# Optimization experiments

Hardware: AMD Instinct MI355X
Metric: run time of the kernel (lower is better)

The kernel has to match this reference:

```python
import jax, jax.numpy as jnp
import numpy as np
from jax import lax

B, S, D, H = 512, 120, 216, 1024
MAX_LEN = 24


def setup_inputs() -> dict:
    key = jax.random.key(0)
    ks = jax.random.split(key, 8)
    u = lambda k, shape: jax.random.uniform(k, shape, jnp.float32, -0.08, 0.08)  # init_weights
    return {
        "src": jax.random.normal(ks[0], (B, S, D), jnp.float32),
        "W_ih": u(ks[1], (4 * H, D)),
        "W_hh": u(ks[2], (4 * H, H)),
        "b_ih": u(ks[3], (4 * H,)),
        "b_hh": u(ks[4], (4 * H,)),
        "W_out": u(ks[5], (D, H)),
        "b_out": u(ks[6], (D,)),
        "max_len": MAX_LEN,
    }


def _lstm_cell(x, h, c, W_ih, W_hh, b):
    # PyTorch gate order: i, f, g, o
    gates = x @ W_ih.T + h @ W_hh.T + b  # (B, 4H)
    i, f, g, o = jnp.split(gates, 4, axis=-1)
    c_new = jax.nn.sigmoid(f) * c + jax.nn.sigmoid(i) * jnp.tanh(g)
    h_new = jax.nn.sigmoid(o) * jnp.tanh(c_new)
    return h_new, c_new


def reference(src, W_ih, W_hh, b_ih, b_hh, W_out, b_out, max_len):
    # Eval-mode forward: dropout off; encoder teacher-forced over src;
    b = b_ih + b_hh
    src_t = jnp.swapaxes(src, 0, 1)  # (S, B, D)
    Bsz = src.shape[0]
    Hd = W_hh.shape[1]
    h0 = jnp.zeros((Bsz, Hd), src.dtype)
    c0 = jnp.zeros((Bsz, Hd), src.dtype)

    def enc_step(carry, x_t):
        h, c = carry
        h, c = _lstm_cell(x_t, h, c, W_ih, W_hh, b)
        return (h, c), None

    (h, c), _ = lax.scan(enc_step, (h0, c0), src_t)

    def dec_step(carry, _):
        h, c, inp = carry
        h, c = _lstm_cell(inp, h, c, W_ih, W_hh, b)
        y = h @ W_out.T + b_out  # project_to_output
        return (h, c, y), y

    (_, _, _), ys = lax.scan(dec_step, (h, c, src_t[-1]), None, length=max_len)
    return jnp.swapaxes(ys, 0, 1)  # (B, max_len, D)
```

## Files before the change

kernel.cpp:

```cpp
#include <hip/hip_runtime.h>
#include <cstdint>
#include <cstddef>

#define B_SZ 512
#define S_SZ 120
#define D_SZ 216
#define H_SZ 1024
#define NG   4096
#define DP   256
#define TMAX 24

#define BM 64
#define BN 128
#define BK 64

using bf16_t = __bf16;
using bf16x8 = __attribute__((ext_vector_type(8))) __bf16;
using f32x4  = __attribute__((ext_vector_type(4))) float;

__device__ __forceinline__ void gload16(const void* g, void* l) {
  __builtin_amdgcn_global_load_lds(
      (const __attribute__((address_space(1))) void*)g,
      (__attribute__((address_space(3))) void*)l, 16, 0, 0);
}

__device__ __forceinline__ float fsigmoid(float x) {
  x = fminf(fmaxf(x, -30.f), 30.f);
  return 1.f / (1.f + __expf(-x));
}
__device__ __forceinline__ float ftanh(float x) {
  x = fminf(fmaxf(x, -15.f), 15.f);
  float e = __expf(2.f * x);
  return (e - 1.f) / (e + 1.f);
}

struct __align__(16) Smem {
  union {
    bf16_t bufs[2][6 * 64 * 64];
    struct { char pad[49152]; float gate[64 * 129]; } g;
  };
};


template <int EPI, int N1, int N2>
__global__ __launch_bounds__(256, 1) void gemm_step(
    const bf16_t* __restrict__ A1, int sA1,
    const bf16_t* __restrict__ A2, int sA2,
    const bf16_t* __restrict__ Wsw,
    const float* __restrict__ bias,
    float* __restrict__ cbuf, bf16_t* __restrict__ hout,
    const float* __restrict__ addm, bf16_t* __restrict__ outb,
    float* __restrict__ outf)
{
  constexpr int NTOT = N1 + N2;
  constexpr int KB   = NTOT * 2;
  constexpr int C0 = NTOT < 4 ? NTOT : 4;
  constexpr int R0 = NTOT - C0;
  constexpr int C1 = R0 < 6 ? R0 : 6;
  constexpr int R1 = R0 - C1;
  constexpr int C2 = R1 < 6 ? R1 : 6;
  constexpr int C3 = R1 - C2;
  static_assert(C3 <= 6, "chunk overflow");

  __shared__ Smem sm;
  const int t    = threadIdx.x;
  const int m0   = blockIdx.y * BM;
  const int n0   = blockIdx.x * BN;
  const int lane = t & 63;
  const int wv   = t >> 6;
  const int fr   = lane & 15;
  const int fq   = lane >> 4;

  f32x4 acc[4][2] = {};

  float bias2[2] = {0.f, 0.f};
  if (EPI == 1 || EPI == 3) {
#pragma unroll
    for (int nj = 0; nj < 2; ++nj) {
      int col = n0 + wv * 32 + nj * 16 + fr;
      bias2[nj] = (EPI == 3 && col >= D_SZ) ? 0.f : bias[col];
    }
  }

  auto stageChunk = [&](int ci, int kst, int csz) {
    const bf16_t* Ap; int sA; int kloc;
    if (ci == 0 && N1 > 0) { Ap = A1; sA = sA1; kloc = 0; }
    else                   { Ap = A2; sA = sA2; kloc = kst - N1 * BK; }
    char* base = (char*)&sm.bufs[ci & 1][0];
    const int row8 = t >> 3;
    const int c16s = (t & 7);
#pragma unroll
    for (int half = 0; half < 2; ++half) {
      int row = half * 32 + row8;
      int gc  = (c16s ^ (row & 7)) * 8;
      const bf16_t* ga = Ap + (size_t)(m0 + row) * sA + kloc + gc;
      char* ldst = base + (half * 32 + wv * 8) * 128;
      for (int seg = 0; seg < csz; ++seg)
        gload16(ga + seg * 64, ldst + seg * 8192);
    }
  };

  const int nb0 = (n0 >> 4) + wv * 2;
  auto loadB = [&](int it, bf16x8* Bv) {
#pragma unroll
    for (int nj = 0; nj < 2; ++nj)
#pragma unroll
      for (int kk = 0; kk < 2; ++kk)
        Bv[nj * 2 + kk] = *(const bf16x8*)((const char*)Wsw +
            ((size_t)((nb0 + nj) * KB + it * 2 + kk) * 64 + lane) * 16);
  };

  auto compute = [&](const bf16x8* Bv, int bufi, int seg) {
    const char* base = (const char*)&sm.bufs[bufi][0] + seg * 8192;
#pragma unroll
    for (int kk = 0; kk < 2; ++kk)
#pragma unroll
      for (int mi = 0; mi < 4; ++mi) {
        int row = mi * 16 + fr;
        bf16x8 av = *(const bf16x8*)(base + row * 128 +
                                     (((kk * 4 + fq) ^ (row & 7)) * 16));
        acc[mi][0] = __builtin_amdgcn_mfma_f32_16x16x32_bf16(av, Bv[kk],     acc[mi][0], 0, 0, 0);
        acc[mi][1] = __builtin_amdgcn_mfma_f32_16x16x32_bf16(av, Bv[2 + kk], acc[mi][1], 0, 0, 0);
      }
  };

  bf16x8 Bv[2][4];
  loadB(0, Bv[0]);
  stageChunk(0, 0, C0);
  __syncthreads();
  if (C1 > 0) stageChunk(1, C0 * BK, C1);
#pragma unroll
  for (int i = 0; i < C0; ++i) {
    if (i + 1 < NTOT) loadB(i + 1, Bv[(i + 1) & 1]);
    compute(Bv[i & 1], 0, i);
  }
  if (C1 > 0) {
    __syncthreads();
    if (C2 > 0) stageChunk(2, (C0 + C1) * BK, C2);
#pragma unroll
    for (int i = 0; i < C1; ++i) {
      int it = C0 + i;
      if (it + 1 < NTOT) loadB(it + 1, Bv[(it + 1) & 1]);
      compute(Bv[it & 1], 1, i);
    }
  }
  if (C2 > 0) {
    __syncthreads();
    if (C3 > 0) stageChunk(3, (C0 + C1 + C2) * BK, C3);
#pragma unroll
    for (int i = 0; i < C2; ++i) {
      int it = C0 + C1 + i;
      if (it + 1 < NTOT) loadB(it + 1, Bv[(it + 1) & 1]);
      compute(Bv[it & 1], 0, i);
    }
  }
  if (C3 > 0) {
    __syncthreads();
#pragma unroll
    for (int i = 0; i < C3; ++i) {
      int it = C0 + C1 + C2 + i;
      if (it + 1 < NTOT) loadB(it + 1, Bv[(it + 1) & 1]);
      compute(Bv[it & 1], 1, i);
    }
  }
  __syncthreads();

  if (EPI == 1) {
#pragma unroll
    for (int mi = 0; mi < 4; ++mi)
#pragma unroll
      for (int nj = 0; nj < 2; ++nj)
#pragma unroll
        for (int v = 0; v < 4; ++v) {
          int row = mi * 16 + fq * 4 + v;
          int col = wv * 32 + nj * 16 + fr;
          sm.g.gate[row * 129 + col] = acc[mi][nj][v] + bias2[nj];
        }
    __syncthreads();
    const int u0 = n0 >> 2;
#pragma unroll
    for (int itc = 0; itc < 8; ++itc) {
      int ci = itc * 256 + t;
      int brw = ci >> 5;
      int ju  = ci & 31;
      const float* gp = &sm.g.gate[brw * 129 + ju * 4];
      float iv = fsigmoid(gp[0]);
      float fv = fsigmoid(gp[1]);
      float gv = ftanh(gp[2]);
      float ov = fsigmoid(gp[3]);
      size_t cix = (size_t)(m0 + brw) * H_SZ + (u0 + ju);
      float cn = fv * cbuf[cix] + iv * gv;
      cbuf[cix] = cn;
      hout[cix] = (bf16_t)(ov * ftanh(cn));
    }
  }

  if (EPI == 2) {
#pragma unroll
    for (int mi = 0; mi < 4; ++mi)
#pragma unroll
      for (int nj = 0; nj < 2; ++nj)
#pragma unroll
        for (int v = 0; v < 4; ++v) {
          int row = mi * 16 + fq * 4 + v;
          int col = wv * 32 + nj * 16 + fr;
          int gr = m0 + row, gc = n0 + col;
          int orig = (gr & 3) * H_SZ + (gr >> 2);
          sm.g.gate[row * 129 + col] = acc[mi][nj][v] + addm[(size_t)orig * H_SZ + gc];
        }
    __syncthreads();
#pragma unroll
    for (int q = 0; q < 4; ++q) {
      int c = q * 256 + t;
      int nbl = c >> 8, kbl = (c >> 6) & 3, l2 = c & 63;
      int nloc = nbl * 16 + (l2 & 15);
      int kloc = kbl * 32 + (l2 >> 4) * 8;
      const float* gp = &sm.g.gate[nloc * 129 + kloc];
      bf16x8 v;
#pragma unroll
      for (int j = 0; j < 8; ++j) v[j] = (bf16_t)gp[j];
      size_t chunk = (size_t)(((m0 >> 4) + nbl) * 32 + (n0 >> 5) + kbl) * 64 + l2;
      *(bf16x8*)(outb + chunk * 8) = v;
    }
  }

  if (EPI == 3) {
#pragma unroll
    for (int mi = 0; mi < 4; ++mi)
#pragma unroll
      for (int nj = 0; nj < 2; ++nj)
#pragma unroll
        for (int v = 0; v < 4; ++v) {
          int m = m0 + mi * 16 + fq * 4 + v;
          int n = n0 + wv * 32 + nj * 16 + fr;
          if (n < D_SZ) {
            outf[((size_t)(m & 511) * TMAX + (m >> 9)) * D_SZ + n] =
                acc[mi][nj][v] + bias2[nj];
          }
        }
  }
}

__global__ void k_convert_src(const float* __restrict__ src, bf16_t* __restrict__ dst) {
  int idx = blockIdx.x * 256 + threadIdx.x;
  int total = S_SZ * B_SZ * DP;
  if (idx >= total) return;
  int d = idx % DP;
  int r = idx / DP;
  int b = r % B_SZ;
  int tt = r / B_SZ;
  float v = (d < D_SZ) ? src[((size_t)b * S_SZ + tt) * D_SZ + d] : 0.f;
  dst[idx] = (bf16_t)v;
}

__global__ void k_build_wcat_sw(const float* __restrict__ Wih, const float* __restrict__ Whh,
                                bf16_t* __restrict__ out) {
  int c = blockIdx.x * 256 + threadIdx.x;
  if (c >= 256 * 40 * 64) return;
  int l = c & 63;
  int kb = (c >> 6) % 40;
  int nb = c / (40 * 64);
  int n = nb * 16 + (l & 15);
  int k0 = kb * 32 + (l >> 4) * 8;
  int o = (n & 3) * H_SZ + (n >> 2);
  bf16x8 v;
#pragma unroll
  for (int j = 0; j < 8; ++j) {
    int k = k0 + j;
    float x = (k < D_SZ) ? Wih[(size_t)o * D_SZ + k]
            : (k < DP ? 0.f : Whh[(size_t)o * H_SZ + (k - DP)]);
    v[j] = (bf16_t)x;
  }
  *(bf16x8*)(out + (size_t)c * 8) = v;
}

__global__ void k_build_woutt_sw(const float* __restrict__ Wout, bf16_t* __restrict__ out) {
  int c = blockIdx.x * 256 + threadIdx.x;
  if (c >= 64 * 8 * 64) return;
  int l = c & 63;
  int kb = (c >> 6) % 8;
  int nb = c / (8 * 64);
  int n = nb * 16 + (l & 15);
  int k0 = kb * 32 + (l >> 4) * 8;
  bf16x8 v;
#pragma unroll
  for (int j = 0; j < 8; ++j) {
    int k = k0 + j;
    v[j] = (bf16_t)((k < D_SZ) ? Wout[(size_t)k * H_SZ + n] : 0.f);
  }
  *(bf16x8*)(out + (size_t)c * 8) = v;
}

__global__ void k_build_wout_sw(const float* __restrict__ Wout, bf16_t* __restrict__ out) {
  int c = blockIdx.x * 256 + threadIdx.x;
  if (c >= 16 * 32 * 64) return;
  int l = c & 63;
  int kb = (c >> 6) % 32;
  int nb = c / (32 * 64);
  int n = nb * 16 + (l & 15);
  int k0 = kb * 32 + (l >> 4) * 8;
  bf16x8 v;
#pragma unroll
  for (int j = 0; j < 8; ++j)
    v[j] = (bf16_t)((n < D_SZ) ? Wout[(size_t)n * H_SZ + k0 + j] : 0.f);
  *(bf16x8*)(out + (size_t)c * 8) = v;
}

__global__ void k_build_wihre(const float* __restrict__ Wih, bf16_t* __restrict__ out) {
  int c = blockIdx.x * 256 + threadIdx.x;
  if (c >= 4096 * 32) return;
  int r = c >> 5;
  int k0 = (c & 31) * 8;
  int o = (r & 3) * H_SZ + (r >> 2);
  bf16x8 v;
#pragma unroll
  for (int j = 0; j < 8; ++j) {
    int k = k0 + j;
    v[j] = (bf16_t)((k < D_SZ) ? Wih[(size_t)o * D_SZ + k] : 0.f);
  }
  *(bf16x8*)(out + (size_t)c * 8) = v;
}

__global__ void k_build_bias(const float* __restrict__ bih, const float* __restrict__ bhh,
                             const float* __restrict__ Wih, const float* __restrict__ bout,
                             float* __restrict__ biasE, float* __restrict__ biasD) {
  int r = blockIdx.x * 256 + threadIdx.x;
  if (r >= NG) return;
  int o = (r & 3) * H_SZ + (r >> 2);
  float be = bih[o] + bhh[o];
  biasE[r] = be;
  float s = 0.f;
  const float* wr = Wih + (size_t)o * D_SZ;
  for (int d = 0; d < D_SZ; ++d) s += wr[d] * bout[d];
  biasD[r] = be + s;
}

extern "C" void kernel_launch(void* const* d_in, const int* in_sizes, int n_in,
                              void* d_out, int out_size, void* d_ws, size_t ws_size,
                              hipStream_t stream) {
  const float* src  = (const float*)d_in[0];
  const float* Wih  = (const float*)d_in[1];
  const float* Whh  = (const float*)d_in[2];
  const float* bih  = (const float*)d_in[3];
  const float* bhh  = (const float*)d_in[4];
  const float* Wout = (const float*)d_in[5];
  const float* bout = (const float*)d_in[6];

  char* ws = (char*)d_ws;
  size_t off = 0;
  auto alloc = [&](size_t bytes) {
    void* p = ws + off;
    off = (off + bytes + 255) & ~(size_t)255;
    return p;
  };
  bf16_t* srcbf  = (bf16_t*)alloc((size_t)S_SZ * B_SZ * DP * 2);
  bf16_t* WcatSw = (bf16_t*)alloc((size_t)256 * 40 * 64 * 16);
  bf16_t* WdecSw = (bf16_t*)alloc((size_t)NG * H_SZ * 2);
  bf16_t* WouttSw= (bf16_t*)alloc((size_t)64 * 8 * 64 * 16);
  bf16_t* WoutSw = (bf16_t*)alloc((size_t)16 * 32 * 64 * 16);
  bf16_t* WihRe  = (bf16_t*)alloc((size_t)NG * DP * 2);
  float*  biasE  = (float*)alloc((size_t)NG * 4);
  float*  biasD  = (float*)alloc((size_t)NG * 4);
  float*  cbuf   = (float*)alloc((size_t)B_SZ * H_SZ * 4);
  bf16_t* hP0    = (bf16_t*)alloc((size_t)B_SZ * H_SZ * 2);
  bf16_t* hP1    = (bf16_t*)alloc((size_t)B_SZ * H_SZ * 2);
  bf16_t* Hs     = (bf16_t*)alloc((size_t)TMAX * B_SZ * H_SZ * 2);

  hipMemsetAsync(cbuf, 0, (size_t)B_SZ * H_SZ * 4, stream);
  hipMemsetAsync(hP0, 0, (size_t)B_SZ * H_SZ * 2, stream);

  k_convert_src<<<(S_SZ * B_SZ * DP + 255) / 256, 256, 0, stream>>>(src, srcbf);
  k_build_wcat_sw<<<(256 * 40 * 64 + 255) / 256, 256, 0, stream>>>(Wih, Whh, WcatSw);
  k_build_woutt_sw<<<(64 * 8 * 64 + 255) / 256, 256, 0, stream>>>(Wout, WouttSw);
  k_build_wout_sw<<<(16 * 32 * 64 + 255) / 256, 256, 0, stream>>>(Wout, WoutSw);
  k_build_wihre<<<(4096 * 32 + 255) / 256, 256, 0, stream>>>(Wih, WihRe);
  k_build_bias<<<(NG + 255) / 256, 256, 0, stream>>>(bih, bhh, Wih, bout, biasE, biasD);

  gemm_step<2, 4, 0><<<dim3(H_SZ / BN, NG / BM), 256, 0, stream>>>(
      WihRe, DP, nullptr, 0, WouttSw, nullptr,
      nullptr, nullptr, Whh, WdecSw, nullptr);

  const bf16_t* hprev = hP0;
  for (int s = 0; s < 144; ++s) {
    bf16_t* hnext;
    if (s < 120) hnext = (hprev == hP0) ? hP1 : hP0;
    else         hnext = Hs + (size_t)(s - 120) * B_SZ * H_SZ;
    if (s <= 120) {
      int xi = (s <= 119) ? s : 119;
      gemm_step<1, 4, 16><<<dim3(NG / BN, B_SZ / BM), 256, 0, stream>>>(
          srcbf + (size_t)xi * B_SZ * DP, DP, hprev, H_SZ,
          WcatSw, biasE, cbuf, hnext, nullptr, nullptr, nullptr);
    } else {
      gemm_step<1, 0, 16><<<dim3(NG / BN, B_SZ / BM), 256, 0, stream>>>(
          nullptr, 0, hprev, H_SZ,
          WdecSw, biasD, cbuf, hnext, nullptr, nullptr, nullptr);
    }
    hprev = hnext;
  }

  gemm_step<3, 0, 16><<<dim3(2, (TMAX * B_SZ) / BM), 256, 0, stream>>>(
      nullptr, 0, Hs, H_SZ, WoutSw, bout,
      nullptr, nullptr, nullptr, nullptr, (float*)d_out);
}
```

Measured before the change: 2.023 ms.

## Replace per-step LSTM launches with persistent kernel using per-row-group barriers

Replaces the 144 per-timestep gemm_step launches with a single persistent kernel of 256 blocks. Blocks sync through atomic counters per batch-row group, so each block waits only on the 32 blocks producing its rows of h. The cell state now stays in registers instead of a global cbuf, and the x-projection for the next step is issued before the wait on h, so it overlaps the barrier. This removes launch overhead and global c traffic. In exchange it depends on all 256 blocks being co-resident, or the spin-waits deadlock, and it adds spin-wait and fence latency.

```diff
diff --git a/kernel.cpp b/kernel.cpp
--- a/kernel.cpp
+++ b/kernel.cpp
@@ -42,13 +42,176 @@
 };
 
 
+__global__ __launch_bounds__(256, 1) void lstm_persist(
+    const bf16_t* __restrict__ srcbf,
+    const bf16_t* __restrict__ WcatSw,
+    const bf16_t* __restrict__ WdecSw,
+    const float* __restrict__ biasE,
+    const float* __restrict__ biasD,
+    bf16_t* __restrict__ hP0, bf16_t* __restrict__ hP1,
+    bf16_t* __restrict__ Hs,
+    int* __restrict__ bars)
+{
+  __shared__ Smem sm;
+  const int t    = threadIdx.x;
+  const int nt   = blockIdx.x;
+  const int gI   = blockIdx.y;
+  const int m0   = gI * BM;
+  const int n0   = nt * BN;
+  const int lane = t & 63;
+  const int wv   = t >> 6;
+  const int fr   = lane & 15;
+  const int fq   = lane >> 4;
+  const int u0   = n0 >> 2;
+  const size_t BH = (size_t)B_SZ * H_SZ;
+
+  float bE[2], bD[2];
+#pragma unroll
+  for (int nj = 0; nj < 2; ++nj) {
+    int col = n0 + wv * 32 + nj * 16 + fr;
+    bE[nj] = biasE[col];
+    bD[nj] = biasD[col];
+  }
+
+  float creg[8];
+#pragma unroll
+  for (int i = 0; i < 8; ++i) creg[i] = 0.f;
+
+  const int nb0  = (n0 >> 4) + wv * 2;
+  const int row8 = t >> 3;
+  const int c16s = t & 7;
+
+  auto stageA = [&](const bf16_t* Ap, int sA, int buf, int k0, int nseg) {
+    char* base = (char*)&sm.bufs[0][0] + buf * 49152;
+#pragma unroll
+    for (int half = 0; half < 2; ++half) {
+      int row = half * 32 + row8;
+      int gc  = (c16s ^ (row & 7)) * 8;
+      const bf16_t* ga = Ap + (size_t)(m0 + row) * sA + k0 + gc;
+      char* ldst = base + (half * 32 + wv * 8) * 128;
+      for (int seg = 0; seg < nseg; ++seg)
+        gload16(ga + seg * 64, ldst + seg * 8192);
+    }
+  };
+
+  for (int s = 0; s < 144; ++s) {
+    const bool enc = (s <= 120);
+    const int  KBs = enc ? 40 : 32;
+    const bf16_t* Wb0 = (enc ? WcatSw : WdecSw) + (size_t)nb0 * KBs * 512;
+    const bf16_t* Wb1 = Wb0 + (size_t)KBs * 512;
+    const float*  b2  = enc ? bE : bD;
+    bf16_t* hw = (s < 120) ? ((s & 1) ? hP1 : hP0) : Hs + (size_t)(s - 120) * BH;
+    const bf16_t* hr = (s == 0) ? nullptr
+                     : (s - 1 < 120) ? (((s - 1) & 1) ? hP1 : hP0)
+                                     : Hs + (size_t)(s - 1 - 120) * BH;
+
+    f32x4 acc[4][2] = {};
+    bf16x8 Bv[2][4];
+
+    auto loadB = [&](int kb, bf16x8* B) {
+      B[0] = *(const bf16x8*)(Wb0 + (size_t)kb * 512 + lane * 8);
+      B[1] = *(const bf16x8*)(Wb0 + (size_t)(kb + 1) * 512 + lane * 8);
+      B[2] = *(const bf16x8*)(Wb1 + (size_t)kb * 512 + lane * 8);
+      B[3] = *(const bf16x8*)(Wb1 + (size_t)(kb + 1) * 512 + lane * 8);
+    };
+    auto compute = [&](int buf, int seg, const bf16x8* B) {
+      const char* base = (const char*)&sm.bufs[0][0] + buf * 49152 + seg * 8192;
+#pragma unroll
+      for (int kk = 0; kk < 2; ++kk)
+#pragma unroll
+        for (int mi = 0; mi < 4; ++mi) {
+          int row = mi * 16 + fr;
+          bf16x8 av = *(const bf16x8*)(base + row * 128 +
+                                       (((kk * 4 + fq) ^ (row & 7)) * 16));
+          acc[mi][0] = __builtin_amdgcn_mfma_f32_16x16x32_bf16(av, B[kk],     acc[mi][0], 0, 0, 0);
+          acc[mi][1] = __builtin_amdgcn_mfma_f32_16x16x32_bf16(av, B[2 + kk], acc[mi][1], 0, 0, 0);
+        }
+    };
+
+    int it = 0;
+    if (enc) {
+      int xi = (s <= 119) ? s : 119;
+      const bf16_t* As = srcbf + (size_t)xi * B_SZ * DP;
+      stageA(As, DP, 0, 0, 4);
+      loadB(0, Bv[0]);
+      __syncthreads();
+#pragma unroll
+      for (int i = 0; i < 4; ++i, ++it) {
+        loadB(2 * (it + 1), Bv[(it + 1) & 1]);
+        compute(0, i, Bv[it & 1]);
+      }
+    }
+    if (s > 0) {
+      if (t == 0) {
+        while (__hip_atomic_load(&bars[(s - 1) * 8 + gI], __ATOMIC_RELAXED,
+                                 __HIP_MEMORY_SCOPE_AGENT) < 32)
+          __builtin_amdgcn_s_sleep(2);
+      }
+      __syncthreads();
+      __threadfence();
+      stageA(hr, H_SZ, 1, 0, 6);
+      __syncthreads();
+      stageA(hr, H_SZ, 0, 384, 6);
+      if (!enc) loadB(2 * it, Bv[it & 1]);
+#pragma unroll
+      for (int i = 0; i < 6; ++i, ++it) {
+        loadB(2 * (it + 1), Bv[(it + 1) & 1]);
+        compute(1, i, Bv[it & 1]);
+      }
+      __syncthreads();
+      stageA(hr, H_SZ, 1, 768, 4);
+#pragma unroll
+      for (int i = 0; i < 6; ++i, ++it) {
+        loadB(2 * (it + 1), Bv[(it + 1) & 1]);
+        compute(0, i, Bv[it & 1]);
+      }
+      __syncthreads();
+#pragma unroll
+      for (int i = 0; i < 4; ++i, ++it) {
+        if (i < 3) loadB(2 * (it + 1), Bv[(it + 1) & 1]);
+        compute(1, i, Bv[it & 1]);
+      }
+    }
+
+    __syncthreads();
+#pragma unroll
+    for (int mi = 0; mi < 4; ++mi)
+#pragma unroll
+      for (int nj = 0; nj < 2; ++nj)
+#pragma unroll
+        for (int v = 0; v < 4; ++v) {
+          int row = mi * 16 + fq * 4 + v;
+          int col = wv * 32 + nj * 16 + fr;
+          sm.g.gate[row * 129 + col] = acc[mi][nj][v] + b2[nj];
+        }
+    __syncthreads();
+#pragma unroll
+    for (int itc = 0; itc < 8; ++itc) {
+      int brw = itc * 8 + (t >> 5);
+      int ju  = t & 31;
+      const float* gp = &sm.g.gate[brw * 129 + ju * 4];
+      float iv = fsigmoid(gp[0]);
+      float fv = fsigmoid(gp[1]);
+      float gv = ftanh(gp[2]);
+      float ov = fsigmoid(gp[3]);
+      float cn = fv * creg[itc] + iv * gv;
+      creg[itc] = cn;
+      hw[(size_t)(m0 + brw) * H_SZ + (u0 + ju)] = (bf16_t)(ov * ftanh(cn));
+    }
+    __threadfence();
+    __syncthreads();
+    if (t == 0)
+      __hip_atomic_fetch_add(&bars[s * 8 + gI], 1, __ATOMIC_RELAXED,
+                             __HIP_MEMORY_SCOPE_AGENT);
+  }
+}
+
 template <int EPI, int N1, int N2>
 __global__ __launch_bounds__(256, 1) void gemm_step(
     const bf16_t* __restrict__ A1, int sA1,
     const bf16_t* __restrict__ A2, int sA2,
     const bf16_t* __restrict__ Wsw,
     const float* __restrict__ bias,
-    float* __restrict__ cbuf, bf16_t* __restrict__ hout,
     const float* __restrict__ addm, bf16_t* __restrict__ outb,
     float* __restrict__ outf)
 {
@@ -74,11 +237,11 @@
   f32x4 acc[4][2] = {};
 
   float bias2[2] = {0.f, 0.f};
-  if (EPI == 1 || EPI == 3) {
+  if (EPI == 3) {
 #pragma unroll
     for (int nj = 0; nj < 2; ++nj) {
       int col = n0 + wv * 32 + nj * 16 + fr;
-      bias2[nj] = (EPI == 3 && col >= D_SZ) ? 0.f : bias[col];
+      bias2[nj] = (col >= D_SZ) ? 0.f : bias[col];
     }
   }
 
@@ -101,13 +264,13 @@
   };
 
   const int nb0 = (n0 >> 4) + wv * 2;
-  auto loadB = [&](int it, bf16x8* Bv) {
+  auto loadB = [&](int itq, bf16x8* Bv) {
 #pragma unroll
     for (int nj = 0; nj < 2; ++nj)
 #pragma unroll
       for (int kk = 0; kk < 2; ++kk)
         Bv[nj * 2 + kk] = *(const bf16x8*)((const char*)Wsw +
-            ((size_t)((nb0 + nj) * KB + it * 2 + kk) * 64 + lane) * 16);
+            ((size_t)((nb0 + nj) * KB + itq * 2 + kk) * 64 + lane) * 16);
   };
 
   auto compute = [&](const bf16x8* Bv, int bufi, int seg) {
@@ -139,9 +302,9 @@
     if (C2 > 0) stageChunk(2, (C0 + C1) * BK, C2);
 #pragma unroll
     for (int i = 0; i < C1; ++i) {
-      int it = C0 + i;
-      if (it + 1 < NTOT) loadB(it + 1, Bv[(it + 1) & 1]);
-      compute(Bv[it & 1], 1, i);
+      int itq = C0 + i;
+      if (itq + 1 < NTOT) loadB(itq + 1, Bv[(itq + 1) & 1]);
+      compute(Bv[itq & 1], 1, i);
     }
   }
   if (C2 > 0) {
@@ -149,51 +312,21 @@
     if (C3 > 0) stageChunk(3, (C0 + C1 + C2) * BK, C3);
 #pragma unroll
     for (int i = 0; i < C2; ++i) {
-      int it = C0 + C1 + i;
-      if (it + 1 < NTOT) loadB(it + 1, Bv[(it + 1) & 1]);
-      compute(Bv[it & 1], 0, i);
+      int itq = C0 + C1 + i;
+      if (itq + 1 < NTOT) loadB(itq + 1, Bv[(itq + 1) & 1]);
+      compute(Bv[itq & 1], 0, i);
     }
   }
   if (C3 > 0) {
     __syncthreads();
 #pragma unroll
     for (int i = 0; i < C3; ++i) {
-      int it = C0 + C1 + C2 + i;
-      if (it + 1 < NTOT) loadB(it + 1, Bv[(it + 1) & 1]);
-      compute(Bv[it & 1], 1, i);
+      int itq = C0 + C1 + C2 + i;
+      if (itq + 1 < NTOT) loadB(itq + 1, Bv[(itq + 1) & 1]);
+      compute(Bv[itq & 1], 1, i);
     }
   }
   __syncthreads();
-
-  if (EPI == 1) {
-#pragma unroll
-    for (int mi = 0; mi < 4; ++mi)
-#pragma unroll
-      for (int nj = 0; nj < 2; ++nj)
-#pragma unroll
-        for (int v = 0; v < 4; ++v) {
-          int row = mi * 16 + fq * 4 + v;
-          int col = wv * 32 + nj * 16 + fr;
-          sm.g.gate[row * 129 + col] = acc[mi][nj][v] + bias2[nj];
-        }
-    __syncthreads();
-    const int u0 = n0 >> 2;
-#pragma unroll
-    for (int itc = 0; itc < 8; ++itc) {
-      int ci = itc * 256 + t;
-      int brw = ci >> 5;
-      int ju  = ci & 31;
-      const float* gp = &sm.g.gate[brw * 129 + ju * 4];
-      float iv = fsigmoid(gp[0]);
-      float fv = fsigmoid(gp[1]);
-      float gv = ftanh(gp[2]);
-      float ov = fsigmoid(gp[3]);
-      size_t cix = (size_t)(m0 + brw) * H_SZ + (u0 + ju);
-      float cn = fv * cbuf[cix] + iv * gv;
-      cbuf[cix] = cn;
-      hout[cix] = (bf16_t)(ov * ftanh(cn));
-    }
-  }
 
   if (EPI == 2) {
 #pragma unroll
@@ -361,13 +494,12 @@
   bf16_t* WihRe  = (bf16_t*)alloc((size_t)NG * DP * 2);
   float*  biasE  = (float*)alloc((size_t)NG * 4);
   float*  biasD  = (float*)alloc((size_t)NG * 4);
-  float*  cbuf   = (float*)alloc((size_t)B_SZ * H_SZ * 4);
   bf16_t* hP0    = (bf16_t*)alloc((size_t)B_SZ * H_SZ * 2);
   bf16_t* hP1    = (bf16_t*)alloc((size_t)B_SZ * H_SZ * 2);
   bf16_t* Hs     = (bf16_t*)alloc((size_t)TMAX * B_SZ * H_SZ * 2);
-
-  hipMemsetAsync(cbuf, 0, (size_t)B_SZ * H_SZ * 4, stream);
-  hipMemsetAsync(hP0, 0, (size_t)B_SZ * H_SZ * 2, stream);
+  int*    bars   = (int*)alloc((size_t)144 * 8 * 4);
+
+  hipMemsetAsync(bars, 0, (size_t)144 * 8 * 4, stream);
 
   k_convert_src<<<(S_SZ * B_SZ * DP + 255) / 256, 256, 0, stream>>>(src, srcbf);
   k_build_wcat_sw<<<(256 * 40 * 64 + 255) / 256, 256, 0, stream>>>(Wih, Whh, WcatSw);
@@ -377,28 +509,11 @@
   k_build_bias<<<(NG + 255) / 256, 256, 0, stream>>>(bih, bhh, Wih, bout, biasE, biasD);
 
   gemm_step<2, 4, 0><<<dim3(H_SZ / BN, NG / BM), 256, 0, stream>>>(
-      WihRe, DP, nullptr, 0, WouttSw, nullptr,
-      nullptr, nullptr, Whh, WdecSw, nullptr);
-
-  const bf16_t* hprev = hP0;
-  for (int s = 0; s < 144; ++s) {
-    bf16_t* hnext;
-    if (s < 120) hnext = (hprev == hP0) ? hP1 : hP0;
-    else         hnext = Hs + (size_t)(s - 120) * B_SZ * H_SZ;
-    if (s <= 120) {
-      int xi = (s <= 119) ? s : 119;
-      gemm_step<1, 4, 16><<<dim3(NG / BN, B_SZ / BM), 256, 0, stream>>>(
-          srcbf + (size_t)xi * B_SZ * DP, DP, hprev, H_SZ,
-          WcatSw, biasE, cbuf, hnext, nullptr, nullptr, nullptr);
-    } else {
-      gemm_step<1, 0, 16><<<dim3(NG / BN, B_SZ / BM), 256, 0, stream>>>(
-          nullptr, 0, hprev, H_SZ,
-          WdecSw, biasD, cbuf, hnext, nullptr, nullptr, nullptr);
-    }
-    hprev = hnext;
-  }
+      WihRe, DP, nullptr, 0, WouttSw, nullptr, Whh, WdecSw, nullptr);
+
+  lstm_persist<<<dim3(32, 8), 256, 0, stream>>>(
+      srcbf, WcatSw, WdecSw, biasE, biasD, hP0, hP1, Hs, bars);
 
   gemm_step<3, 0, 16><<<dim3(2, (TMAX * B_SZ) / BM), 256, 0, stream>>>(
-      nullptr, 0, Hs, H_SZ, WoutSw, bout,
-      nullptr, nullptr, nullptr, nullptr, (float*)d_out);
-}
+      nullptr, 0, Hs, H_SZ, WoutSw, bout, nullptr, nullptr, (float*)d_out);
+}
```

Result: slower. 7.308 ms (+261.3%).
